# Optimization experiments

Hardware: AMD Instinct MI355X
Metric: run time of the kernel (lower is better)

## Reference

```python
import jax, jax.numpy as jnp
import numpy as np

N, P, B, F, M, L, H = 10000, 25000, 8, 16, 32, 2, 2  # nodes, edge-pairs, batch, feats, MLP_feats, n_layers, MLP_layers


def setup_inputs() -> dict:
    key = jax.random.key(0)
    rng = np.random.default_rng(0)
    u = rng.integers(0, N, size=P)
    v = rng.integers(0, N, size=P)
    # E = 2P+1: forward pairs, reversed pairs, one fixed edge (matches cat([eff,-eff,fixed]))
    src = jnp.asarray(np.concatenate([u, v, [0]]), dtype=jnp.int32)
    dst = jnp.asarray(np.concatenate([v, u, [0]]), dtype=jnp.int32)
    ks = jax.random.split(key, 14)
    w = lambda k, shape, fan: jax.random.normal(k, shape, jnp.float32) * (fan ** -0.5)
    b = lambda k, shape: jax.random.normal(k, shape, jnp.float32) * 0.01
    return {
        'h': jax.random.normal(ks[0], (B, N, F), jnp.float32),
        # per-edge-pair (interactive) MLP params, stacked over n_layers L
        'Wi0': w(ks[1], (L, P, 2 * F, M), 2 * F),
        'Wih': w(ks[2], (L, H, P, M, M), M),
        'Wiout': w(ks[3], (L, P, M, F), M),
        'bi0': b(ks[4], (L, P, 1, M)),
        'bih': b(ks[5], (L, H, P, 1, M)),
        'biout': b(ks[6], (L, P, 1, F)),
        # shared (fixed-edge) MLP params
        'Wf0': w(ks[7], (L, 1, 2 * F, M), 2 * F),
        'Wfh': w(ks[8], (L, H, 1, M, M), M),
        'Wfout': w(ks[9], (L, 1, M, F), M),
        'bf0': b(ks[10], (L, 1, 1, M)),
        'bfh': b(ks[11], (L, H, 1, 1, M)),
        'bfout': b(ks[12], (L, 1, 1, F)),
        'src': src,
        'dst': dst,
    }


def _edge_mlp(x, W0, Wh, Wout, b0, bh, bout):
    # x: [P,B,2F]; batched per-edge MLP with SiLU hidden activations
    y = jax.nn.silu(jnp.einsum('pbf,pfm->pbm', x, W0) + b0)
    for i in range(Wh.shape[0]):
        y = jax.nn.silu(jnp.einsum('pbf,pfm->pbm', y, Wh[i]) + bh[i])
    return jnp.einsum('pbf,pfm->pbm', y, Wout) + bout


def reference(h, Wi0, Wih, Wiout, bi0, bih, biout, Wf0, Wfh, Wfout, bf0, bfh, bfout, src, dst):
    n_nodes = h.shape[1]
    E = src.shape[0]
    p = (E - 1) // 2
    x = jnp.transpose(h, (1, 0, 2))  # [N,B,F] (torch permute(1,0,2))
    for l in range(Wi0.shape[0]):
        # gather only the edges actually used: first P pairs + the final fixed edge
        e_eff = jnp.concatenate([x[dst[:p]], x[src[:p]]], axis=-1)   # [P,B,2F]
        e_fix = jnp.concatenate([x[dst[-1:]], x[src[-1:]]], axis=-1)  # [1,B,2F]
        eff = _edge_mlp(e_eff, Wi0[l], Wih[l], Wiout[l], bi0[l], bih[l], biout[l])
        fx = _edge_mlp(e_fix, Wf0[l], Wfh[l], Wfout[l], bf0[l], bfh[l], bfout[l])
        msgs = jnp.concatenate([eff, -eff, fx], axis=0)  # [E,B,F]
        x = jax.ops.segment_sum(msgs, dst, num_segments=n_nodes)  # sum-reduce onto dst nodes
    return jnp.transpose(x, (1, 0, 2))  # back to [B,N,F]
```

## Files before the change

### kernel.cpp

```cpp
#include <hip/hip_runtime.h>

#define BB 8
#define FF 16
#define MM 32
#define TF 32
#define ROW 40

__device__ __forceinline__ float silu_f(float x) {
    return x / (1.0f + __expf(-x));
}

__device__ __forceinline__ float4 dense32(const float* __restrict__ Wp, int rstride,
                                          const float a[TF], float4 acc) {
#pragma unroll
    for (int k = 0; k < TF; ++k) {
        const float4 wv = *(const float4*)(Wp + k * rstride);
        acc.x += a[k] * wv.x;
        acc.y += a[k] * wv.y;
        acc.z += a[k] * wv.z;
        acc.w += a[k] * wv.w;
    }
    return acc;
}

__device__ __forceinline__ void load_row(const float* arow, float a[TF]) {
#pragma unroll
    for (int c = 0; c < 8; ++c) {
        const float4 t = *(const float4*)(arow + 4 * c);
        a[4 * c + 0] = t.x;
        a[4 * c + 1] = t.y;
        a[4 * c + 2] = t.z;
        a[4 * c + 3] = t.w;
    }
}

extern "C" __global__ void __launch_bounds__(256) gnn_edge_kernel(
    const float* __restrict__ x_in, float* __restrict__ x_out,
    const float* __restrict__ Wi0, const float* __restrict__ Wih,
    const float* __restrict__ Wiout, const float* __restrict__ bi0,
    const float* __restrict__ bih, const float* __restrict__ biout,
    const float* __restrict__ Wf0, const float* __restrict__ Wfh,
    const float* __restrict__ Wfout, const float* __restrict__ bf0,
    const float* __restrict__ bfh, const float* __restrict__ bfout,
    const int* __restrict__ src, const int* __restrict__ dst,
    int P, int E, int H,
    long in_ns, long in_bs,
    long out_ns, long out_bs)
{
    __shared__ float act[4][BB * ROW];

    const int w    = threadIdx.x >> 6;
    const int lane = threadIdx.x & 63;
    const int b    = lane >> 3;
    const int lg   = lane & 7;
    const int cg   = lg & 3;

    const bool isFixed = (blockIdx.x == (int)gridDim.x - 1);
    if (isFixed && w != 0) return;

    int p, nd, ns;
    const float *W0p, *Whp, *Woutp, *b0p, *bhp, *boutp;
    long whstride, bhstride;
    if (isFixed) {
        W0p = Wf0; Whp = Wfh; Woutp = Wfout;
        b0p = bf0; bhp = bfh; boutp = bfout;
        whstride = (long)(MM * MM);
        bhstride = (long)MM;
        nd = dst[E - 1];
        ns = src[E - 1];
    } else {
        p = blockIdx.x * 4 + w;
        if (p >= P) return;
        W0p   = Wi0   + (long)p * (TF * MM);
        Whp   = Wih   + (long)p * (MM * MM);
        Woutp = Wiout + (long)p * (MM * FF);
        b0p   = bi0   + (long)p * MM;
        bhp   = bih   + (long)p * MM;
        boutp = biout + (long)p * FF;
        whstride = (long)P * (MM * MM);
        bhstride = (long)P * MM;
        nd = dst[p];
        ns = src[p];
    }

    float* arow = &act[w][b * ROW];

    {
        const int   gnode = (lg < 4) ? nd : ns;
        const float* gp = x_in + (long)gnode * in_ns + (long)b * in_bs + cg * 4;
        const float4 g = *(const float4*)gp;
        *(float4*)(arow + ((lg < 4) ? 0 : FF) + cg * 4) = g;
    }

    float a[TF];
    float4 r;

    load_row(arow, a);
    r = dense32(W0p + lg * 4, MM, a, *(const float4*)(b0p + lg * 4));
    r.x = silu_f(r.x); r.y = silu_f(r.y); r.z = silu_f(r.z); r.w = silu_f(r.w);
    *(float4*)(arow + lg * 4) = r;

    for (int i = 0; i < H; ++i) {
        load_row(arow, a);
        r = dense32(Whp + (long)i * whstride + lg * 4, MM, a,
                    *(const float4*)(bhp + (long)i * bhstride + lg * 4));
        r.x = silu_f(r.x); r.y = silu_f(r.y); r.z = silu_f(r.z); r.w = silu_f(r.w);
        *(float4*)(arow + lg * 4) = r;
    }

    load_row(arow, a);
    r = dense32(Woutp + cg * 4, FF, a, *(const float4*)(boutp + cg * 4));

    const bool pos = (lg < 4);
    if (isFixed && !pos) return;
    const int   node = pos ? nd : ns;
    const float s    = pos ? 1.0f : -1.0f;
    float* op = x_out + (long)node * out_ns + (long)b * out_bs + cg * 4;
    atomicAdd(op + 0, s * r.x);
    atomicAdd(op + 1, s * r.y);
    atomicAdd(op + 2, s * r.z);
    atomicAdd(op + 3, s * r.w);
}

extern "C" void kernel_launch(void* const* d_in, const int* in_sizes, int n_in,
                              void* d_out, int out_size, void* d_ws, size_t ws_size,
                              hipStream_t stream)
{
    const float* h     = (const float*)d_in[0];
    const float* Wi0   = (const float*)d_in[1];
    const float* Wih   = (const float*)d_in[2];
    const float* Wiout = (const float*)d_in[3];
    const float* bi0   = (const float*)d_in[4];
    const float* bih   = (const float*)d_in[5];
    const float* biout = (const float*)d_in[6];
    const float* Wf0   = (const float*)d_in[7];
    const float* Wfh   = (const float*)d_in[8];
    const float* Wfout = (const float*)d_in[9];
    const float* bf0   = (const float*)d_in[10];
    const float* bfh   = (const float*)d_in[11];
    const float* bfout = (const float*)d_in[12];
    const int*   src   = (const int*)d_in[13];
    const int*   dst   = (const int*)d_in[14];

    const int E = in_sizes[13];
    const int P = (E - 1) / 2;
    const int N = in_sizes[0] / (BB * FF);
    const int L = (int)((long)in_sizes[1] / ((long)P * TF * MM));
    const int H = (int)((long)in_sizes[2] / ((long)L * P * MM * MM));

    float* ws0 = (float*)d_ws;
    float* ws1 = ws0 + (long)N * BB * FF;

    const int blocksE = (P + 3) / 4;
    dim3 grid(blocksE + 1), block(256);

    for (int l = 0; l < L; ++l) {
        const float* xin;
        long ins_n, ins_b;
        if (l == 0) { xin = h; ins_n = FF; ins_b = (long)N * FF; }
        else        { xin = (l % 2 == 1) ? ws0 : ws1; ins_n = BB * FF; ins_b = FF; }

        float* xout;
        long outs_n, outs_b;
        if (l == L - 1) { xout = (float*)d_out; outs_n = FF; outs_b = (long)N * FF; }
        else            { xout = (l % 2 == 0) ? ws0 : ws1; outs_n = BB * FF; outs_b = FF; }

        hipMemsetAsync(xout, 0, (size_t)N * BB * FF * sizeof(float), stream);

        gnn_edge_kernel<<<grid, block, 0, stream>>>(
            xin, xout,
            Wi0   + (long)l * P * TF * MM,
            Wih   + (long)l * H * P * MM * MM,
            Wiout + (long)l * P * MM * FF,
            bi0   + (long)l * P * MM,
            bih   + (long)l * H * P * MM,
            biout + (long)l * P * FF,
            Wf0   + (long)l * TF * MM,
            Wfh   + (long)l * H * MM * MM,
            Wfout + (long)l * MM * FF,
            bf0   + (long)l * MM,
            bfh   + (long)l * H * MM,
            bfout + (long)l * FF,
            src, dst, P, E, H,
            ins_n, ins_b, outs_n, outs_b);
    }
}
```

Measured before the change: 891.2 us.

## Replace atomic scatter with CSR-based gather of buffered edge messages

Edge MLP outputs are written to a workspace message buffer, and a CSR index (count, scan, fill) built per call lets one wave per node sum its incoming messages without atomics. This removes float atomicAdd contention and the per-layer memset. The cost is extra kernels, including a single-wave serial scan over all nodes, plus a round trip of messages through memory. If the workspace is too small, the edges are processed in chunks, with one gather pass per chunk that scans every node's full entry list.

```diff
diff --git a/kernel.cpp b/kernel.cpp
--- a/kernel.cpp
+++ b/kernel.cpp
@@ -5,6 +5,7 @@
 #define MM 32
 #define TF 32
 #define ROW 40
+#define MROW (BB * FF)
 
 __device__ __forceinline__ float silu_f(float x) {
     return x / (1.0f + __expf(-x));
@@ -32,6 +33,167 @@
         a[4 * c + 2] = t.z;
         a[4 * c + 3] = t.w;
     }
+}
+
+extern "C" __global__ void __launch_bounds__(256) gnn_edge_msgs(
+    const float* __restrict__ x_in, float* __restrict__ msg,
+    const float* __restrict__ Wi0, const float* __restrict__ Wih,
+    const float* __restrict__ Wiout, const float* __restrict__ bi0,
+    const float* __restrict__ bih, const float* __restrict__ biout,
+    const float* __restrict__ Wf0, const float* __restrict__ Wfh,
+    const float* __restrict__ Wfout, const float* __restrict__ bf0,
+    const float* __restrict__ bfh, const float* __restrict__ bfout,
+    const int* __restrict__ src, const int* __restrict__ dst,
+    int P, int E, int H, int e0, int e1,
+    long in_ns, long in_bs)
+{
+    __shared__ float act[4][BB * ROW];
+
+    const int w    = threadIdx.x >> 6;
+    const int lane = threadIdx.x & 63;
+    const int b    = lane >> 3;
+    const int lg   = lane & 7;
+    const int cg   = lg & 3;
+
+    const int p = e0 + blockIdx.x * 4 + w;
+    if (p >= e1) return;
+    const bool isFixed = (p == P);
+
+    int nd, ns;
+    const float *W0p, *Whp, *Woutp, *b0p, *bhp, *boutp;
+    long whstride, bhstride;
+    if (isFixed) {
+        W0p = Wf0; Whp = Wfh; Woutp = Wfout;
+        b0p = bf0; bhp = bfh; boutp = bfout;
+        whstride = (long)(MM * MM);
+        bhstride = (long)MM;
+        nd = dst[E - 1];
+        ns = src[E - 1];
+    } else {
+        W0p   = Wi0   + (long)p * (TF * MM);
+        Whp   = Wih   + (long)p * (MM * MM);
+        Woutp = Wiout + (long)p * (MM * FF);
+        b0p   = bi0   + (long)p * MM;
+        bhp   = bih   + (long)p * MM;
+        boutp = biout + (long)p * FF;
+        whstride = (long)P * (MM * MM);
+        bhstride = (long)P * MM;
+        nd = dst[p];
+        ns = src[p];
+    }
+    const long mrow = (long)(p - e0) * MROW;
+
+    float* arow = &act[w][b * ROW];
+
+    {
+        const int   gnode = (lg < 4) ? nd : ns;
+        const float* gp = x_in + (long)gnode * in_ns + (long)b * in_bs + cg * 4;
+        const float4 g = *(const float4*)gp;
+        *(float4*)(arow + ((lg < 4) ? 0 : FF) + cg * 4) = g;
+    }
+
+    float a[TF];
+    float4 r;
+
+    load_row(arow, a);
+    r = dense32(W0p + lg * 4, MM, a, *(const float4*)(b0p + lg * 4));
+    r.x = silu_f(r.x); r.y = silu_f(r.y); r.z = silu_f(r.z); r.w = silu_f(r.w);
+    *(float4*)(arow + lg * 4) = r;
+
+    for (int i = 0; i < H; ++i) {
+        load_row(arow, a);
+        r = dense32(Whp + (long)i * whstride + lg * 4, MM, a,
+                    *(const float4*)(bhp + (long)i * bhstride + lg * 4));
+        r.x = silu_f(r.x); r.y = silu_f(r.y); r.z = silu_f(r.z); r.w = silu_f(r.w);
+        *(float4*)(arow + lg * 4) = r;
+    }
+
+    load_row(arow, a);
+    r = dense32(Woutp + cg * 4, FF, a, *(const float4*)(boutp + cg * 4));
+
+    if (lg < 4) {
+        *(float4*)(msg + mrow + b * FF + cg * 4) = r;
+    }
+}
+
+extern "C" __global__ void __launch_bounds__(256) csr_count_kernel(
+    const int* __restrict__ src, const int* __restrict__ dst,
+    int* __restrict__ cnt, int P, int E)
+{
+    const int e = blockIdx.x * blockDim.x + threadIdx.x;
+    const int total = 2 * P + 1;
+    if (e >= total) return;
+    int node;
+    if (e < P)            node = dst[e];
+    else if (e < 2 * P)   node = src[e - P];
+    else                  node = dst[E - 1];
+    atomicAdd(&cnt[node], 1);
+}
+
+extern "C" __global__ void __launch_bounds__(64) csr_scan_kernel(
+    const int* __restrict__ cnt, int* __restrict__ offs, int N)
+{
+    const int lane = threadIdx.x;
+    int base = 0;
+    for (int i0 = 0; i0 < N; i0 += 64) {
+        const int i = i0 + lane;
+        const int orig = (i < N) ? cnt[i] : 0;
+        int v = orig;
+#pragma unroll
+        for (int d = 1; d < 64; d <<= 1) {
+            const int t = __shfl_up(v, d, 64);
+            if (lane >= d) v += t;
+        }
+        if (i < N) offs[i] = base + v - orig;
+        base += __shfl(v, 63, 64);
+    }
+    if (lane == 0) offs[N] = base;
+}
+
+extern "C" __global__ void __launch_bounds__(256) csr_fill_kernel(
+    const int* __restrict__ src, const int* __restrict__ dst,
+    const int* __restrict__ offs, int* __restrict__ cur,
+    int* __restrict__ entries, int P, int E)
+{
+    const int e = blockIdx.x * blockDim.x + threadIdx.x;
+    const int total = 2 * P + 1;
+    if (e >= total) return;
+    int node, eid, neg;
+    if (e < P)          { node = dst[e];     eid = e;     neg = 0; }
+    else if (e < 2 * P) { node = src[e - P]; eid = e - P; neg = 1; }
+    else                { node = dst[E - 1]; eid = P;     neg = 0; }
+    const int pos = offs[node] + atomicAdd(&cur[node], 1);
+    entries[pos] = (eid << 1) | neg;
+}
+
+extern "C" __global__ void __launch_bounds__(256) gnn_gather_kernel(
+    const float* __restrict__ msg, const int* __restrict__ offs,
+    const int* __restrict__ entries, float* __restrict__ x_out,
+    int N, int e0, int e1, int init, long out_ns, long out_bs)
+{
+    const int wv   = threadIdx.x >> 6;
+    const int lane = threadIdx.x & 63;
+    const int node = blockIdx.x * 4 + wv;
+    if (node >= N) return;
+
+    const int beg = offs[node];
+    const int end = offs[node + 1];
+    const int idx = lane * 2;
+    const int b   = idx >> 4;
+    const int f   = idx & 15;
+
+    float* op = x_out + (long)node * out_ns + (long)b * out_bs + f;
+    float2 acc = init ? make_float2(0.0f, 0.0f) : *(const float2*)op;
+    for (int i = beg; i < end; ++i) {
+        const int ent = entries[i];
+        const int eid = ent >> 1;
+        if (eid < e0 || eid >= e1) continue;
+        const float s = (ent & 1) ? -1.0f : 1.0f;
+        const float2 m = *(const float2*)(msg + (long)(eid - e0) * MROW + idx);
+        acc.x += s * m.x;
+        acc.y += s * m.y;
+    }
+    *(float2*)op = acc;
 }
 
 extern "C" __global__ void __launch_bounds__(256) gnn_edge_kernel(
@@ -44,8 +206,7 @@
     const float* __restrict__ bfh, const float* __restrict__ bfout,
     const int* __restrict__ src, const int* __restrict__ dst,
     int P, int E, int H,
-    long in_ns, long in_bs,
-    long out_ns, long out_bs)
+    long in_ns, long in_bs, long out_ns, long out_bs)
 {
     __shared__ float act[4][BB * ROW];
 
@@ -84,7 +245,6 @@
     }
 
     float* arow = &act[w][b * ROW];
-
     {
         const int   gnode = (lg < 4) ? nd : ns;
         const float* gp = x_in + (long)gnode * in_ns + (long)b * in_bs + cg * 4;
@@ -148,40 +308,106 @@
     const int L = (int)((long)in_sizes[1] / ((long)P * TF * MM));
     const int H = (int)((long)in_sizes[2] / ((long)L * P * MM * MM));
 
-    float* ws0 = (float*)d_ws;
-    float* ws1 = ws0 + (long)N * BB * FF;
-
-    const int blocksE = (P + 3) / 4;
-    dim3 grid(blocksE + 1), block(256);
-
-    for (int l = 0; l < L; ++l) {
-        const float* xin;
-        long ins_n, ins_b;
-        if (l == 0) { xin = h; ins_n = FF; ins_b = (long)N * FF; }
-        else        { xin = (l % 2 == 1) ? ws0 : ws1; ins_n = BB * FF; ins_b = FF; }
-
-        float* xout;
-        long outs_n, outs_b;
-        if (l == L - 1) { xout = (float*)d_out; outs_n = FF; outs_b = (long)N * FF; }
-        else            { xout = (l % 2 == 0) ? ws0 : ws1; outs_n = BB * FF; outs_b = FF; }
-
-        hipMemsetAsync(xout, 0, (size_t)N * BB * FF * sizeof(float), stream);
-
-        gnn_edge_kernel<<<grid, block, 0, stream>>>(
-            xin, xout,
-            Wi0   + (long)l * P * TF * MM,
-            Wih   + (long)l * H * P * MM * MM,
-            Wiout + (long)l * P * MM * FF,
-            bi0   + (long)l * P * MM,
-            bih   + (long)l * H * P * MM,
-            biout + (long)l * P * FF,
-            Wf0   + (long)l * TF * MM,
-            Wfh   + (long)l * H * MM * MM,
-            Wfout + (long)l * MM * FF,
-            bf0   + (long)l * MM,
-            bfh   + (long)l * H * MM,
-            bfout + (long)l * FF,
-            src, dst, P, E, H,
-            ins_n, ins_b, outs_n, outs_b);
-    }
-}
+    const long NBF   = (long)N * BB * FF;
+    const int  total = 2 * P + 1;
+
+    float* wsf = (float*)d_ws;
+    long off = 0;
+    float* ws0 = wsf + off; if (L >= 2) off += NBF;
+    float* ws1 = wsf + off; if (L >= 3) off += NBF;
+    long int_words = (long)2 * N + (N + 1) + total;
+    int* cnt     = (int*)(wsf + off);
+    int* cur     = cnt + N;
+    int* offs    = cur + N;
+    int* entries = offs + (N + 1);
+    const long off_msg = off + ((int_words + 3) & ~3L);
+    float* msg = wsf + off_msg;
+
+    const long ws_floats = (long)(ws_size / 4);
+    const long rows_cap  = (ws_floats > off_msg) ? (ws_floats - off_msg) / MROW : 0;
+    const long min_rows  = ((long)P + 1 + 15) / 16;
+    const bool fast      = (rows_cap >= min_rows) && (rows_cap >= 1);
+
+    const int blocksN = (N + 3) / 4;
+
+    if (fast) {
+        const int C  = (int)(((long)P + 1 + rows_cap - 1) / rows_cap);
+        const int pc = (P + 1 + C - 1) / C;
+
+        hipMemsetAsync(cnt, 0, (size_t)(2 * N) * sizeof(int), stream);
+        csr_count_kernel<<<dim3((total + 255) / 256), dim3(256), 0, stream>>>(src, dst, cnt, P, E);
+        csr_scan_kernel<<<dim3(1), dim3(64), 0, stream>>>(cnt, offs, N);
+        csr_fill_kernel<<<dim3((total + 255) / 256), dim3(256), 0, stream>>>(src, dst, offs, cur, entries, P, E);
+
+        for (int l = 0; l < L; ++l) {
+            const float* xin;
+            long ins_n, ins_b;
+            if (l == 0) { xin = h; ins_n = FF; ins_b = (long)N * FF; }
+            else        { xin = (l % 2 == 1) ? ws0 : ws1; ins_n = BB * FF; ins_b = FF; }
+
+            float* xout;
+            long outs_n, outs_b;
+            if (l == L - 1) { xout = (float*)d_out; outs_n = FF; outs_b = (long)N * FF; }
+            else            { xout = (l % 2 == 0) ? ws0 : ws1; outs_n = BB * FF; outs_b = FF; }
+
+            for (int c = 0; c < C; ++c) {
+                const int e0 = c * pc;
+                const int e1 = (e0 + pc < P + 1) ? (e0 + pc) : (P + 1);
+                const int blocksE = (e1 - e0 + 3) / 4;
+
+                gnn_edge_msgs<<<dim3(blocksE), dim3(256), 0, stream>>>(
+                    xin, msg,
+                    Wi0   + (long)l * P * TF * MM,
+                    Wih   + (long)l * H * P * MM * MM,
+                    Wiout + (long)l * P * MM * FF,
+                    bi0   + (long)l * P * MM,
+                    bih   + (long)l * H * P * MM,
+                    biout + (long)l * P * FF,
+                    Wf0   + (long)l * TF * MM,
+                    Wfh   + (long)l * H * MM * MM,
+                    Wfout + (long)l * MM * FF,
+                    bf0   + (long)l * MM,
+                    bfh   + (long)l * H * MM,
+                    bfout + (long)l * FF,
+                    src, dst, P, E, H, e0, e1,
+                    ins_n, ins_b);
+
+                gnn_gather_kernel<<<dim3(blocksN), dim3(256), 0, stream>>>(
+                    msg, offs, entries, xout, N, e0, e1, (c == 0) ? 1 : 0,
+                    outs_n, outs_b);
+            }
+        }
+    } else {
+        const int blocksE = (P + 3) / 4;
+        for (int l = 0; l < L; ++l) {
+            const float* xin;
+            long ins_n, ins_b;
+            if (l == 0) { xin = h; ins_n = FF; ins_b = (long)N * FF; }
+            else        { xin = (l % 2 == 1) ? ws0 : ws1; ins_n = BB * FF; ins_b = FF; }
+
+            float* xout;
+            long outs_n, outs_b;
+            if (l == L - 1) { xout = (float*)d_out; outs_n = FF; outs_b = (long)N * FF; }
+            else            { xout = (l % 2 == 0) ? ws0 : ws1; outs_n = BB * FF; outs_b = FF; }
+
+            hipMemsetAsync(xout, 0, (size_t)NBF * sizeof(float), stream);
+
+            gnn_edge_kernel<<<dim3(blocksE + 1), dim3(256), 0, stream>>>(
+                xin, xout,
+                Wi0   + (long)l * P * TF * MM,
+                Wih   + (long)l * H * P * MM * MM,
+                Wiout + (long)l * P * MM * FF,
+                bi0   + (long)l * P * MM,
+                bih   + (long)l * H * P * MM,
+                biout + (long)l * P * FF,
+                Wf0   + (long)l * TF * MM,
+                Wfh   + (long)l * H * MM * MM,
+                Wfout + (long)l * MM * FF,
+                bf0   + (long)l * MM,
+                bfh   + (long)l * H * MM,
+                bfout + (long)l * FF,
+                src, dst, P, E, H,
+                ins_n, ins_b, outs_n, outs_b);
+        }
+    }
+}
```

New measurement: 970.4 us. 1.09x slower.
